# Performance work log

Hardware: AMD Instinct MI355X
Metric: run time of the kernel (lower is better)

Reference implementation:

```python
import jax, jax.numpy as jnp
import numpy as np

B, S, H, I = 2, 2048, 4096, 11008  # batch, seq, hidden_size, intermediate_size (Llama-7B)


def setup_inputs() -> dict:
    key = jax.random.key(0)
    ks = jax.random.split(key, 11)
    # int8 activations and weights (SmoothQuant W8A8)
    hidden_states = jax.random.randint(ks[0], (B, S, H), -128, 128, dtype=jnp.int8)
    w_gate = jax.random.randint(ks[1], (I, H), -128, 128, dtype=jnp.int8)
    w_up = jax.random.randint(ks[2], (I, H), -128, 128, dtype=jnp.int8)
    w_down = jax.random.randint(ks[3], (H, I), -128, 128, dtype=jnp.int8)
    # dequant scales (alpha = input_scale * weight_scale), small positive
    gate_a = jax.random.uniform(ks[4], (1,), dtype=jnp.float32) * 1e-4 + 1e-5
    up_a = jax.random.uniform(ks[5], (1,), dtype=jnp.float32) * 1e-4 + 1e-5
    down_a = jax.random.uniform(ks[6], (1,), dtype=jnp.float32) * 1e-4 + 1e-5
    # fp32 biases
    gate_b = jax.random.normal(ks[7], (I,), dtype=jnp.float32) * 0.01
    up_b = jax.random.normal(ks[8], (I,), dtype=jnp.float32) * 0.01
    down_b = jax.random.normal(ks[9], (H,), dtype=jnp.float32) * 0.01
    # requantization scale for down_proj input
    down_scale = jax.random.uniform(ks[10], (1,), dtype=jnp.float32) * 0.05 + 0.01
    return {
        "hidden_states": hidden_states,
        "w_gate": w_gate, "w_up": w_up, "w_down": w_down,
        "gate_a": gate_a, "gate_b": gate_b,
        "up_a": up_a, "up_b": up_b,
        "down_a": down_a, "down_b": down_b,
        "down_scale": down_scale,
    }


def _i8_gemm(x_i8, w_i8):
    return jnp.einsum("bsk,nk->bsn", x_i8, w_i8, preferred_element_type=jnp.int32)


def reference(hidden_states, w_gate, w_up, w_down,
              gate_a, gate_b, up_a, up_b, down_a, down_b, down_scale):
    # gate_proj: W8A8 GEMM -> dequant (alpha) + fp32 bias -> fused SiLU
    g = _i8_gemm(hidden_states, w_gate).astype(jnp.float32) * gate_a[0] + gate_b
    gate_out = g * jax.nn.sigmoid(g)  # SiLU
    # up_proj: W8A8 GEMM -> dequant + fp32 bias
    up_out = _i8_gemm(hidden_states, w_up).astype(jnp.float32) * up_a[0] + up_b
    inter = gate_out * up_out
    # requantize to int8 for down_proj input
    q = jnp.clip(jnp.round(inter / down_scale[0]), -128, 127).astype(jnp.int8)
    # down_proj: W8A8 GEMM -> dequant + fp32 bias
    down_out = _i8_gemm(q, w_down).astype(jnp.float32) * down_a[0] + down_b
    return down_out  # [B, S, H] fp32
```

## Files before the change

### kernel.cpp

```cpp
#include <hip/hip_runtime.h>
#include <cstdint>


typedef int v4i  __attribute__((ext_vector_type(4)));
typedef int v16i __attribute__((ext_vector_type(16)));

typedef const void __attribute__((address_space(1)))* gas_ptr;
typedef void __attribute__((address_space(3)))* las_ptr;

static constexpr int M_TOT = 4096;
static constexpr int HDIM  = 4096;
static constexpr int IDIM  = 11008;

#define BM 128
#define BN 128
#define BK 128

__device__ __forceinline__ void pack16(const int* __restrict__ src,
                                       int8_t* __restrict__ dst, int t) {
  const int4* s = (const int4*)(src) + t * 4;
  int4 v0 = s[0], v1 = s[1], v2 = s[2], v3 = s[3];
  int p0 = (v0.x & 0xff) | ((v0.y & 0xff) << 8) | ((v0.z & 0xff) << 16) | (v0.w << 24);
  int p1 = (v1.x & 0xff) | ((v1.y & 0xff) << 8) | ((v1.z & 0xff) << 16) | (v1.w << 24);
  int p2 = (v2.x & 0xff) | ((v2.y & 0xff) << 8) | ((v2.z & 0xff) << 16) | (v2.w << 24);
  int p3 = (v3.x & 0xff) | ((v3.y & 0xff) << 8) | ((v3.z & 0xff) << 16) | (v3.w << 24);
  ((int4*)dst)[t] = make_int4(p0, p1, p2, p3);
}

static constexpr int CX = (M_TOT * HDIM) / 16;
static constexpr int CW = (IDIM * HDIM) / 16;
static constexpr int CTOT = CX + 3 * CW;

__global__ __launch_bounds__(256) void k_pack_all(
    const int* __restrict__ X32, const int* __restrict__ Wg32,
    const int* __restrict__ Wu32, const int* __restrict__ Wd32,
    int8_t* __restrict__ Xp, int8_t* __restrict__ Wgp,
    int8_t* __restrict__ Wup, int8_t* __restrict__ Wdp) {
  int t = blockIdx.x * blockDim.x + threadIdx.x;
  if (t >= CTOT) return;
  if (t < CX)               { pack16(X32,  Xp,  t); return; }
  t -= CX;
  if (t < CW)               { pack16(Wg32, Wgp, t); return; }
  t -= CW;
  if (t < CW)               { pack16(Wu32, Wup, t); return; }
  t -= CW;
  pack16(Wd32, Wdp, t);
}

__device__ __forceinline__ void async_stage_16kb(const int8_t* __restrict__ gbase,
                                                 int ld, int8_t* lds, int tid) {
#pragma unroll
  for (int it = 0; it < 4; ++it) {
    const int chunk = it * 256 + tid;
    const int row   = chunk >> 3;
    const int slot  = chunk & 7;
    const int gch   = slot ^ (row & 7);
    const int8_t* g = gbase + row * ld + gch * 16;
    int8_t* l = lds + chunk * 16;
    __builtin_amdgcn_global_load_lds((gas_ptr)g, (las_ptr)l, 16, 0, 0);
  }
}

__device__ __forceinline__ v4i frag_ld(const int8_t* lds, int row, int kc, int half) {
  const int ch  = kc + half;
  const int sch = ch ^ (row & 7);
  return *(const v4i*)(lds + row * 128 + sch * 16);
}

#define MFMA_I8(a, b, c) __builtin_amdgcn_mfma_i32_32x32x32_i8((a), (b), (c), 0, 0, 0)

__global__ __launch_bounds__(256, 2) void k_gateup(
    const int8_t* __restrict__ X,
    const int8_t* __restrict__ Wg,
    const int8_t* __restrict__ Wu,
    const float* __restrict__ gate_a, const float* __restrict__ gate_b,
    const float* __restrict__ up_a,   const float* __restrict__ up_b,
    const float* __restrict__ down_scale,
    int8_t* __restrict__ Q) {
  __shared__ __align__(16) int8_t sA[BM * BK];
  __shared__ __align__(16) int8_t sG[BN * BK];
  __shared__ __align__(16) int8_t sU[BN * BK];

  const int tid  = threadIdx.x;
  const int lane = tid & 63;
  const int wave = tid >> 6;
  const int wm   = wave >> 1;
  const int wn   = wave & 1;
  const int half = lane >> 5;
  const int ln31 = lane & 31;

  const int m0 = blockIdx.x * BM;
  const int n0 = blockIdx.y * BN;

  const int8_t* Ab = X  + (size_t)m0 * HDIM;
  const int8_t* Gb = Wg + (size_t)n0 * HDIM;
  const int8_t* Ub = Wu + (size_t)n0 * HDIM;

  v16i accG[2][2], accU[2][2];
#pragma unroll
  for (int i = 0; i < 2; ++i)
#pragma unroll
    for (int j = 0; j < 2; ++j)
#pragma unroll
      for (int e = 0; e < 16; ++e) { accG[i][j][e] = 0; accU[i][j][e] = 0; }

  const int rA = wm * 64 + ln31;
  const int rB = wn * 64 + ln31;

  for (int k0 = 0; k0 < HDIM; k0 += BK) {
    async_stage_16kb(Ab + k0, HDIM, sA, tid);
    async_stage_16kb(Gb + k0, HDIM, sG, tid);
    async_stage_16kb(Ub + k0, HDIM, sU, tid);
    __syncthreads();
#pragma unroll
    for (int kc = 0; kc < 8; kc += 2) {
      v4i a0 = frag_ld(sA, rA,      kc, half);
      v4i a1 = frag_ld(sA, rA + 32, kc, half);
      v4i g0 = frag_ld(sG, rB,      kc, half);
      v4i g1 = frag_ld(sG, rB + 32, kc, half);
      v4i u0 = frag_ld(sU, rB,      kc, half);
      v4i u1 = frag_ld(sU, rB + 32, kc, half);
      accG[0][0] = MFMA_I8(a0, g0, accG[0][0]);
      accG[0][1] = MFMA_I8(a0, g1, accG[0][1]);
      accG[1][0] = MFMA_I8(a1, g0, accG[1][0]);
      accG[1][1] = MFMA_I8(a1, g1, accG[1][1]);
      accU[0][0] = MFMA_I8(a0, u0, accU[0][0]);
      accU[0][1] = MFMA_I8(a0, u1, accU[0][1]);
      accU[1][0] = MFMA_I8(a1, u0, accU[1][0]);
      accU[1][1] = MFMA_I8(a1, u1, accU[1][1]);
    }
    __syncthreads();
  }

  const float ga = gate_a[0];
  const float ua = up_a[0];
  const float inv_ds = 1.0f / down_scale[0];

#pragma unroll
  for (int tm = 0; tm < 2; ++tm) {
#pragma unroll
    for (int tn = 0; tn < 2; ++tn) {
      const int n = n0 + wn * 64 + tn * 32 + ln31;
      const float gb = gate_b[n];
      const float ub = up_b[n];
#pragma unroll
      for (int r = 0; r < 16; ++r) {
        const int row_l = (r & 3) + 8 * (r >> 2) + 4 * half;
        const int m = m0 + wm * 64 + tm * 32 + row_l;
        const float g = (float)accG[tm][tn][r] * ga + gb;
        const float u = (float)accU[tm][tn][r] * ua + ub;
        const float sg = g / (1.0f + __expf(-g));
        const float inter = sg * u;
        float qf = rintf(inter * inv_ds);
        qf = fminf(127.0f, fmaxf(-128.0f, qf));
        Q[(size_t)m * IDIM + n] = (int8_t)qf;
      }
    }
  }
}

__global__ __launch_bounds__(256, 2) void k_down(
    const int8_t* __restrict__ Q,
    const int8_t* __restrict__ Wd,
    const float* __restrict__ down_a, const float* __restrict__ down_b,
    float* __restrict__ Out) {
  __shared__ __align__(16) int8_t sA[256 * BK];
  __shared__ __align__(16) int8_t sB[128 * BK];

  const int tid  = threadIdx.x;
  const int lane = tid & 63;
  const int wave = tid >> 6;
  const int wm   = wave >> 1;
  const int wn   = wave & 1;
  const int half = lane >> 5;
  const int ln31 = lane & 31;

  const int m0 = blockIdx.x * 256;
  const int n0 = blockIdx.y * 128;

  const int8_t* Ab = Q  + (size_t)m0 * IDIM;
  const int8_t* Bb = Wd + (size_t)n0 * IDIM;

  v16i acc[4][2];
#pragma unroll
  for (int i = 0; i < 4; ++i)
#pragma unroll
    for (int j = 0; j < 2; ++j)
#pragma unroll
      for (int e = 0; e < 16; ++e) acc[i][j][e] = 0;

  const int rA = wm * 128 + ln31;
  const int rB = wn * 64 + ln31;

  for (int k0 = 0; k0 < IDIM; k0 += BK) {
    async_stage_16kb(Ab + k0, IDIM, sA, tid);
    async_stage_16kb(Ab + (size_t)128 * IDIM + k0, IDIM, sA + 128 * BK, tid);
    async_stage_16kb(Bb + k0, IDIM, sB, tid);
    __syncthreads();
#pragma unroll
    for (int kc = 0; kc < 8; kc += 2) {
      v4i a0 = frag_ld(sA, rA,      kc, half);
      v4i a1 = frag_ld(sA, rA + 32, kc, half);
      v4i a2 = frag_ld(sA, rA + 64, kc, half);
      v4i a3 = frag_ld(sA, rA + 96, kc, half);
      v4i b0 = frag_ld(sB, rB,      kc, half);
      v4i b1 = frag_ld(sB, rB + 32, kc, half);
      acc[0][0] = MFMA_I8(a0, b0, acc[0][0]);
      acc[0][1] = MFMA_I8(a0, b1, acc[0][1]);
      acc[1][0] = MFMA_I8(a1, b0, acc[1][0]);
      acc[1][1] = MFMA_I8(a1, b1, acc[1][1]);
      acc[2][0] = MFMA_I8(a2, b0, acc[2][0]);
      acc[2][1] = MFMA_I8(a2, b1, acc[2][1]);
      acc[3][0] = MFMA_I8(a3, b0, acc[3][0]);
      acc[3][1] = MFMA_I8(a3, b1, acc[3][1]);
    }
    __syncthreads();
  }

  const float da = down_a[0];
#pragma unroll
  for (int tm = 0; tm < 4; ++tm) {
#pragma unroll
    for (int tn = 0; tn < 2; ++tn) {
      const int n = n0 + wn * 64 + tn * 32 + ln31;
      const float db = down_b[n];
#pragma unroll
      for (int r = 0; r < 16; ++r) {
        const int row_l = (r & 3) + 8 * (r >> 2) + 4 * half;
        const int m = m0 + wm * 128 + tm * 32 + row_l;
        Out[(size_t)m * HDIM + n] = (float)acc[tm][tn][r] * da + db;
      }
    }
  }
}

extern "C" void kernel_launch(void* const* d_in, const int* in_sizes, int n_in,
                              void* d_out, int out_size, void* d_ws, size_t ws_size,
                              hipStream_t stream) {
  const int* X32        = (const int*)d_in[0];
  const int* Wg32       = (const int*)d_in[1];
  const int* Wu32       = (const int*)d_in[2];
  const int* Wd32       = (const int*)d_in[3];
  const float* gate_a   = (const float*)d_in[4];
  const float* gate_b   = (const float*)d_in[5];
  const float* up_a     = (const float*)d_in[6];
  const float* up_b     = (const float*)d_in[7];
  const float* down_a   = (const float*)d_in[8];
  const float* down_b   = (const float*)d_in[9];
  const float* down_scale = (const float*)d_in[10];
  float* Out = (float*)d_out;

  const size_t nX = (size_t)M_TOT * HDIM;
  const size_t nW = (size_t)IDIM * HDIM;

  int8_t* Q   = (int8_t*)d_ws;
  int8_t* Xp  = Q   + nW;
  int8_t* Wgp = Xp  + nX;
  int8_t* Wup = Wgp + nW;
  int8_t* Wdp = Wup + nW;

  k_pack_all<<<(CTOT + 255) / 256, 256, 0, stream>>>(X32, Wg32, Wu32, Wd32,
                                                     Xp, Wgp, Wup, Wdp);

  dim3 g1(M_TOT / BM, IDIM / BN);
  k_gateup<<<g1, dim3(256), 0, stream>>>(Xp, Wgp, Wup, gate_a, gate_b, up_a, up_b,
                                         down_scale, Q);
  dim3 g2(M_TOT / 256, HDIM / 128);
  k_down<<<g2, dim3(256), 0, stream>>>(Q, Wdp, down_a, down_b, Out);
}
```

Before: 1.110 ms.

## Rewrite GEMM mainloops with 4-stage async LDS pipeline, 512-thread blocks, grid swizzle

Both int8 GEMM kernels now use 512-thread workgroups with larger tiles (256x128 for gate/up, 256x256 for down), a 4-buffer ring of 64-wide K slices in LDS prefetched three stages ahead, and a new pair-row swizzled LDS layout. Each K slice is split into two halves that interleave issuing the next global-to-LDS loads with MFMA work, with explicit s_waitcnt/s_barrier and setprio around the MFMA bursts. Block ids are remapped through a grid swizzle for L2 locality. The goal is to hide global memory latency and raise MFMA utilisation. The cost is heavier LDS use (128KB per block), more barriers, and the possibility of subtle sync mistakes.

```diff
diff --git a/kernel.cpp b/kernel.cpp
--- a/kernel.cpp
+++ b/kernel.cpp
@@ -12,9 +12,28 @@
 static constexpr int HDIM  = 4096;
 static constexpr int IDIM  = 11008;
 
-#define BM 128
-#define BN 128
-#define BK 128
+#define MFMA_I8(a, b, c) __builtin_amdgcn_mfma_i32_32x32x32_i8((a), (b), (c), 0, 0, 0)
+#define BAR()        asm volatile("s_barrier" ::: "memory")
+#define WAIT_LGKM0() asm volatile("s_waitcnt lgkmcnt(0)" ::: "memory")
+#define WAIT_VM(N)   asm volatile("s_waitcnt vmcnt(" #N ")" ::: "memory")
+#define SETPRIO(P)   __builtin_amdgcn_s_setprio(P)
+
+__device__ __forceinline__ void gload16(const int8_t* g, int8_t* l) {
+  __builtin_amdgcn_global_load_lds((gas_ptr)g, (las_ptr)l, 16, 0, 0);
+}
+
+__device__ __forceinline__ v4i frag64(const int8_t* lds, int row, int c) {
+  const int pair = row >> 1;
+  const int slot = ((c << 1) | (row & 1)) ^ (pair & 7);
+  return *(const v4i*)(lds + pair * 128 + slot * 16);
+}
+
+__device__ __forceinline__ void relmap(int rel, int& row, int& col) {
+  const int pair = rel >> 3;
+  const int sl = (rel & 7) ^ (pair & 7);
+  row = pair * 2 + (sl & 1);
+  col = (sl >> 1) * 16;
+}
 
 __device__ __forceinline__ void pack16(const int* __restrict__ src,
                                        int8_t* __restrict__ dst, int t) {
@@ -47,29 +66,7 @@
   pack16(Wd32, Wdp, t);
 }
 
-__device__ __forceinline__ void async_stage_16kb(const int8_t* __restrict__ gbase,
-                                                 int ld, int8_t* lds, int tid) {
-#pragma unroll
-  for (int it = 0; it < 4; ++it) {
-    const int chunk = it * 256 + tid;
-    const int row   = chunk >> 3;
-    const int slot  = chunk & 7;
-    const int gch   = slot ^ (row & 7);
-    const int8_t* g = gbase + row * ld + gch * 16;
-    int8_t* l = lds + chunk * 16;
-    __builtin_amdgcn_global_load_lds((gas_ptr)g, (las_ptr)l, 16, 0, 0);
-  }
-}
-
-__device__ __forceinline__ v4i frag_ld(const int8_t* lds, int row, int kc, int half) {
-  const int ch  = kc + half;
-  const int sch = ch ^ (row & 7);
-  return *(const v4i*)(lds + row * 128 + sch * 16);
-}
-
-#define MFMA_I8(a, b, c) __builtin_amdgcn_mfma_i32_32x32x32_i8((a), (b), (c), 0, 0, 0)
-
-__global__ __launch_bounds__(256, 2) void k_gateup(
+__global__ __launch_bounds__(512, 2) void k_gateup(
     const int8_t* __restrict__ X,
     const int8_t* __restrict__ Wg,
     const int8_t* __restrict__ Wu,
@@ -77,109 +74,179 @@
     const float* __restrict__ up_a,   const float* __restrict__ up_b,
     const float* __restrict__ down_scale,
     int8_t* __restrict__ Q) {
-  __shared__ __align__(16) int8_t sA[BM * BK];
-  __shared__ __align__(16) int8_t sG[BN * BK];
-  __shared__ __align__(16) int8_t sU[BN * BK];
+  __shared__ __align__(16) int8_t lds8[4 * 32768];
 
   const int tid  = threadIdx.x;
   const int lane = tid & 63;
   const int wave = tid >> 6;
-  const int wm   = wave >> 1;
-  const int wn   = wave & 1;
+  const int wm   = wave >> 2;
+  const int wn   = wave & 3;
   const int half = lane >> 5;
   const int ln31 = lane & 31;
 
-  const int m0 = blockIdx.x * BM;
-  const int n0 = blockIdx.y * BN;
+  const int NB  = IDIM / 128;
+  const int NWG = (M_TOT / 256) * NB;
+  const int id  = blockIdx.x;
+  const int swz = (id & 7) * (NWG >> 3) + (id >> 3);
+  const int m0  = (swz / NB) * 256;
+  const int n0  = (swz % NB) * 128;
 
   const int8_t* Ab = X  + (size_t)m0 * HDIM;
   const int8_t* Gb = Wg + (size_t)n0 * HDIM;
   const int8_t* Ub = Wu + (size_t)n0 * HDIM;
 
-  v16i accG[2][2], accU[2][2];
-#pragma unroll
-  for (int i = 0; i < 2; ++i)
-#pragma unroll
-    for (int j = 0; j < 2; ++j)
-#pragma unroll
-      for (int e = 0; e < 16; ++e) { accG[i][j][e] = 0; accU[i][j][e] = 0; }
-
-  const int rA = wm * 64 + ln31;
-  const int rB = wn * 64 + ln31;
-
-  for (int k0 = 0; k0 < HDIM; k0 += BK) {
-    async_stage_16kb(Ab + k0, HDIM, sA, tid);
-    async_stage_16kb(Gb + k0, HDIM, sG, tid);
-    async_stage_16kb(Ub + k0, HDIM, sU, tid);
-    __syncthreads();
-#pragma unroll
-    for (int kc = 0; kc < 8; kc += 2) {
-      v4i a0 = frag_ld(sA, rA,      kc, half);
-      v4i a1 = frag_ld(sA, rA + 32, kc, half);
-      v4i g0 = frag_ld(sG, rB,      kc, half);
-      v4i g1 = frag_ld(sG, rB + 32, kc, half);
-      v4i u0 = frag_ld(sU, rB,      kc, half);
-      v4i u1 = frag_ld(sU, rB + 32, kc, half);
-      accG[0][0] = MFMA_I8(a0, g0, accG[0][0]);
-      accG[0][1] = MFMA_I8(a0, g1, accG[0][1]);
-      accG[1][0] = MFMA_I8(a1, g0, accG[1][0]);
-      accG[1][1] = MFMA_I8(a1, g1, accG[1][1]);
-      accU[0][0] = MFMA_I8(a0, u0, accU[0][0]);
-      accU[0][1] = MFMA_I8(a0, u1, accU[0][1]);
-      accU[1][0] = MFMA_I8(a1, u0, accU[1][0]);
-      accU[1][1] = MFMA_I8(a1, u1, accU[1][1]);
-    }
-    __syncthreads();
+  int r0, c0, r1, c1;
+  relmap(tid, r0, c0);
+  relmap(tid + 512, r1, c1);
+  const size_t offA0 = (size_t)r0 * HDIM + c0;
+  const size_t offA1 = (size_t)r1 * HDIM + c1;
+  const size_t offW  = offA0;
+  const int ldsA0 = tid * 16;
+  const int ldsA1 = (tid + 512) * 16;
+  const int ldsG  = 16384 + tid * 16;
+  const int ldsU  = 24576 + tid * 16;
+
+  v16i accG[4], accU[4];
+#pragma unroll
+  for (int i = 0; i < 4; ++i)
+#pragma unroll
+    for (int e = 0; e < 16; ++e) { accG[i][e] = 0; accU[i][e] = 0; }
+
+  const int rA = wm * 128 + ln31;
+  const int rB = wn * 32 + ln31;
+
+#pragma unroll
+  for (int pt = 0; pt < 3; ++pt) {
+    int8_t* sb = &lds8[pt * 32768];
+    const size_t ks = (size_t)pt * 64;
+    gload16(Ab + ks + offA0, sb + ldsA0);
+    gload16(Ab + ks + offA1, sb + ldsA1);
+    gload16(Gb + ks + offW,  sb + ldsG);
+    gload16(Ub + ks + offW,  sb + ldsU);
+  }
+  WAIT_VM(8);
+  BAR();
+
+  const int NT = HDIM / 64;
+  for (int t = 0; t < NT; ++t) {
+    const int8_t* bufA = &lds8[(t & 3) * 32768];
+    const int8_t* bufG = bufA + 16384;
+    const int8_t* bufU = bufA + 24576;
+    int8_t* sb = &lds8[((t + 3) & 3) * 32768];
+    const size_t ks = (size_t)(t + 3) * 64;
+    const bool st = (t + 3 < NT);
+
+    {
+      v4i a0 = frag64(bufA, rA,      half);
+      v4i a1 = frag64(bufA, rA + 32, half);
+      v4i a2 = frag64(bufA, rA + 64, half);
+      v4i a3 = frag64(bufA, rA + 96, half);
+      v4i gg = frag64(bufG, rB, half);
+      v4i uu = frag64(bufU, rB, half);
+      if (st) {
+        gload16(Ab + ks + offA0, sb + ldsA0);
+        gload16(Ab + ks + offA1, sb + ldsA1);
+      }
+      BAR();
+      WAIT_LGKM0();
+      SETPRIO(1);
+      accG[0] = MFMA_I8(a0, gg, accG[0]);
+      accU[0] = MFMA_I8(a0, uu, accU[0]);
+      accG[1] = MFMA_I8(a1, gg, accG[1]);
+      accU[1] = MFMA_I8(a1, uu, accU[1]);
+      accG[2] = MFMA_I8(a2, gg, accG[2]);
+      accU[2] = MFMA_I8(a2, uu, accU[2]);
+      accG[3] = MFMA_I8(a3, gg, accG[3]);
+      accU[3] = MFMA_I8(a3, uu, accU[3]);
+      SETPRIO(0);
+      BAR();
+    }
+    {
+      v4i a0 = frag64(bufA, rA,      2 + half);
+      v4i a1 = frag64(bufA, rA + 32, 2 + half);
+      v4i a2 = frag64(bufA, rA + 64, 2 + half);
+      v4i a3 = frag64(bufA, rA + 96, 2 + half);
+      v4i gg = frag64(bufG, rB, 2 + half);
+      v4i uu = frag64(bufU, rB, 2 + half);
+      if (st) {
+        gload16(Gb + ks + offW, sb + ldsG);
+        gload16(Ub + ks + offW, sb + ldsU);
+      }
+      BAR();
+      WAIT_LGKM0();
+      SETPRIO(1);
+      accG[0] = MFMA_I8(a0, gg, accG[0]);
+      accU[0] = MFMA_I8(a0, uu, accU[0]);
+      accG[1] = MFMA_I8(a1, gg, accG[1]);
+      accU[1] = MFMA_I8(a1, uu, accU[1]);
+      accG[2] = MFMA_I8(a2, gg, accG[2]);
+      accU[2] = MFMA_I8(a2, uu, accU[2]);
+      accG[3] = MFMA_I8(a3, gg, accG[3]);
+      accU[3] = MFMA_I8(a3, uu, accU[3]);
+      SETPRIO(0);
+      if (t + 3 < NT)      { WAIT_VM(8); }
+      else if (t + 2 < NT) { WAIT_VM(4); }
+      else if (t + 1 < NT) { WAIT_VM(0); }
+      BAR();
+    }
   }
 
   const float ga = gate_a[0];
   const float ua = up_a[0];
   const float inv_ds = 1.0f / down_scale[0];
-
-#pragma unroll
-  for (int tm = 0; tm < 2; ++tm) {
-#pragma unroll
-    for (int tn = 0; tn < 2; ++tn) {
-      const int n = n0 + wn * 64 + tn * 32 + ln31;
-      const float gb = gate_b[n];
-      const float ub = up_b[n];
-#pragma unroll
-      for (int r = 0; r < 16; ++r) {
-        const int row_l = (r & 3) + 8 * (r >> 2) + 4 * half;
-        const int m = m0 + wm * 64 + tm * 32 + row_l;
-        const float g = (float)accG[tm][tn][r] * ga + gb;
-        const float u = (float)accU[tm][tn][r] * ua + ub;
-        const float sg = g / (1.0f + __expf(-g));
-        const float inter = sg * u;
-        float qf = rintf(inter * inv_ds);
-        qf = fminf(127.0f, fmaxf(-128.0f, qf));
-        Q[(size_t)m * IDIM + n] = (int8_t)qf;
-      }
-    }
-  }
-}
-
-__global__ __launch_bounds__(256, 2) void k_down(
-    const int8_t* __restrict__ Q,
+  const int n = n0 + wn * 32 + ln31;
+  const float gb = gate_b[n];
+  const float ub = up_b[n];
+
+#pragma unroll
+  for (int tm = 0; tm < 4; ++tm) {
+#pragma unroll
+    for (int r = 0; r < 16; ++r) {
+      const int row_l = (r & 3) + 8 * (r >> 2) + 4 * half;
+      const int m = m0 + wm * 128 + tm * 32 + row_l;
+      const float g = (float)accG[tm][r] * ga + gb;
+      const float u = (float)accU[tm][r] * ua + ub;
+      const float sg = g / (1.0f + __expf(-g));
+      const float inter = sg * u;
+      float qf = rintf(inter * inv_ds);
+      qf = fminf(127.0f, fmaxf(-128.0f, qf));
+      Q[(size_t)m * IDIM + n] = (int8_t)qf;
+    }
+  }
+}
+
+__global__ __launch_bounds__(512, 2) void k_down(
+    const int8_t* __restrict__ Qm,
     const int8_t* __restrict__ Wd,
     const float* __restrict__ down_a, const float* __restrict__ down_b,
     float* __restrict__ Out) {
-  __shared__ __align__(16) int8_t sA[256 * BK];
-  __shared__ __align__(16) int8_t sB[128 * BK];
+  __shared__ __align__(16) int8_t lds8[4 * 32768];
 
   const int tid  = threadIdx.x;
   const int lane = tid & 63;
   const int wave = tid >> 6;
-  const int wm   = wave >> 1;
-  const int wn   = wave & 1;
+  const int wm   = wave >> 2;
+  const int wn   = wave & 3;
   const int half = lane >> 5;
   const int ln31 = lane & 31;
 
-  const int m0 = blockIdx.x * 256;
-  const int n0 = blockIdx.y * 128;
-
-  const int8_t* Ab = Q  + (size_t)m0 * IDIM;
+  const int id  = blockIdx.x;
+  const int swz = (id & 7) * 32 + (id >> 3);
+  const int m0  = (swz >> 4) * 256;
+  const int n0  = (swz & 15) * 256;
+
+  const int8_t* Ab = Qm + (size_t)m0 * IDIM;
   const int8_t* Bb = Wd + (size_t)n0 * IDIM;
+
+  int r0, c0, r1, c1;
+  relmap(tid, r0, c0);
+  relmap(tid + 512, r1, c1);
+  const size_t off0 = (size_t)r0 * IDIM + c0;
+  const size_t off1 = (size_t)r1 * IDIM + c1;
+  const int ldsA0 = tid * 16;
+  const int ldsA1 = (tid + 512) * 16;
+  const int ldsB0 = 16384 + tid * 16;
+  const int ldsB1 = 16384 + (tid + 512) * 16;
 
   v16i acc[4][2];
 #pragma unroll
@@ -192,19 +259,40 @@
   const int rA = wm * 128 + ln31;
   const int rB = wn * 64 + ln31;
 
-  for (int k0 = 0; k0 < IDIM; k0 += BK) {
-    async_stage_16kb(Ab + k0, IDIM, sA, tid);
-    async_stage_16kb(Ab + (size_t)128 * IDIM + k0, IDIM, sA + 128 * BK, tid);
-    async_stage_16kb(Bb + k0, IDIM, sB, tid);
-    __syncthreads();
-#pragma unroll
-    for (int kc = 0; kc < 8; kc += 2) {
-      v4i a0 = frag_ld(sA, rA,      kc, half);
-      v4i a1 = frag_ld(sA, rA + 32, kc, half);
-      v4i a2 = frag_ld(sA, rA + 64, kc, half);
-      v4i a3 = frag_ld(sA, rA + 96, kc, half);
-      v4i b0 = frag_ld(sB, rB,      kc, half);
-      v4i b1 = frag_ld(sB, rB + 32, kc, half);
+#pragma unroll
+  for (int pt = 0; pt < 3; ++pt) {
+    int8_t* sb = &lds8[pt * 32768];
+    const size_t ks = (size_t)pt * 64;
+    gload16(Ab + ks + off0, sb + ldsA0);
+    gload16(Ab + ks + off1, sb + ldsA1);
+    gload16(Bb + ks + off0, sb + ldsB0);
+    gload16(Bb + ks + off1, sb + ldsB1);
+  }
+  WAIT_VM(8);
+  BAR();
+
+  const int NT = IDIM / 64;
+  for (int t = 0; t < NT; ++t) {
+    const int8_t* bufA = &lds8[(t & 3) * 32768];
+    const int8_t* bufB = bufA + 16384;
+    int8_t* sb = &lds8[((t + 3) & 3) * 32768];
+    const size_t ks = (size_t)(t + 3) * 64;
+    const bool st = (t + 3 < NT);
+
+    {
+      v4i a0 = frag64(bufA, rA,      half);
+      v4i a1 = frag64(bufA, rA + 32, half);
+      v4i a2 = frag64(bufA, rA + 64, half);
+      v4i a3 = frag64(bufA, rA + 96, half);
+      v4i b0 = frag64(bufB, rB,      half);
+      v4i b1 = frag64(bufB, rB + 32, half);
+      if (st) {
+        gload16(Ab + ks + off0, sb + ldsA0);
+        gload16(Ab + ks + off1, sb + ldsA1);
+      }
+      BAR();
+      WAIT_LGKM0();
+      SETPRIO(1);
       acc[0][0] = MFMA_I8(a0, b0, acc[0][0]);
       acc[0][1] = MFMA_I8(a0, b1, acc[0][1]);
       acc[1][0] = MFMA_I8(a1, b0, acc[1][0]);
@@ -213,17 +301,46 @@
       acc[2][1] = MFMA_I8(a2, b1, acc[2][1]);
       acc[3][0] = MFMA_I8(a3, b0, acc[3][0]);
       acc[3][1] = MFMA_I8(a3, b1, acc[3][1]);
-    }
-    __syncthreads();
+      SETPRIO(0);
+      BAR();
+    }
+    {
+      v4i a0 = frag64(bufA, rA,      2 + half);
+      v4i a1 = frag64(bufA, rA + 32, 2 + half);
+      v4i a2 = frag64(bufA, rA + 64, 2 + half);
+      v4i a3 = frag64(bufA, rA + 96, 2 + half);
+      v4i b0 = frag64(bufB, rB,      2 + half);
+      v4i b1 = frag64(bufB, rB + 32, 2 + half);
+      if (st) {
+        gload16(Bb + ks + off0, sb + ldsB0);
+        gload16(Bb + ks + off1, sb + ldsB1);
+      }
+      BAR();
+      WAIT_LGKM0();
+      SETPRIO(1);
+      acc[0][0] = MFMA_I8(a0, b0, acc[0][0]);
+      acc[0][1] = MFMA_I8(a0, b1, acc[0][1]);
+      acc[1][0] = MFMA_I8(a1, b0, acc[1][0]);
+      acc[1][1] = MFMA_I8(a1, b1, acc[1][1]);
+      acc[2][0] = MFMA_I8(a2, b0, acc[2][0]);
+      acc[2][1] = MFMA_I8(a2, b1, acc[2][1]);
+      acc[3][0] = MFMA_I8(a3, b0, acc[3][0]);
+      acc[3][1] = MFMA_I8(a3, b1, acc[3][1]);
+      SETPRIO(0);
+      if (t + 3 < NT)      { WAIT_VM(8); }
+      else if (t + 2 < NT) { WAIT_VM(4); }
+      else if (t + 1 < NT) { WAIT_VM(0); }
+      BAR();
+    }
   }
 
   const float da = down_a[0];
 #pragma unroll
-  for (int tm = 0; tm < 4; ++tm) {
-#pragma unroll
-    for (int tn = 0; tn < 2; ++tn) {
-      const int n = n0 + wn * 64 + tn * 32 + ln31;
-      const float db = down_b[n];
+  for (int tn = 0; tn < 2; ++tn) {
+    const int n = n0 + wn * 64 + tn * 32 + ln31;
+    const float db = down_b[n];
+#pragma unroll
+    for (int tm = 0; tm < 4; ++tm) {
 #pragma unroll
       for (int r = 0; r < 16; ++r) {
         const int row_l = (r & 3) + 8 * (r >> 2) + 4 * half;
@@ -262,9 +379,9 @@
   k_pack_all<<<(CTOT + 255) / 256, 256, 0, stream>>>(X32, Wg32, Wu32, Wd32,
                                                      Xp, Wgp, Wup, Wdp);
 
-  dim3 g1(M_TOT / BM, IDIM / BN);
-  k_gateup<<<g1, dim3(256), 0, stream>>>(Xp, Wgp, Wup, gate_a, gate_b, up_a, up_b,
-                                         down_scale, Q);
-  dim3 g2(M_TOT / 256, HDIM / 128);
-  k_down<<<g2, dim3(256), 0, stream>>>(Q, Wdp, down_a, down_b, Out);
-}
+  k_gateup<<<dim3((M_TOT / 256) * (IDIM / 128)), dim3(512), 0, stream>>>(
+      Xp, Wgp, Wup, gate_a, gate_b, up_a, up_b, down_scale, Q);
+
+  k_down<<<dim3((M_TOT / 256) * (HDIM / 256)), dim3(512), 0, stream>>>(
+      Q, Wdp, down_a, down_b, Out);
+}
```

After: 1.121 ms. No clear change (+0.9%).

## Double-buffer LDS with 512-thread blocks, larger tiles, new swizzle in both GEMMs

Applied to the files above, without the earlier changes.

Both int8 GEMM kernels now use 512-thread blocks with larger output tiles (256x128 for gate/up, 256x256 for down) and double-buffered 128 KB LDS. The next K-tile's global-to-LDS loads are issued before the MFMAs on the current tile. The LDS layout switches to a row-pair XOR swizzle, and MFMA issue priority is raised during compute. The aim is to hide global load latency, raise data reuse per tile and cut bank conflicts, at the cost of heavy LDS use that limits occupancy to one block per CU.

```diff
diff --git a/kernel.cpp b/kernel.cpp
--- a/kernel.cpp
+++ b/kernel.cpp
@@ -12,9 +12,27 @@
 static constexpr int HDIM  = 4096;
 static constexpr int IDIM  = 11008;
 
-#define BM 128
-#define BN 128
-#define BK 128
+#define MFMA_I8(a, b, c) __builtin_amdgcn_mfma_i32_32x32x32_i8((a), (b), (c), 0, 0, 0)
+#define BAR()      asm volatile("s_barrier" ::: "memory")
+#define WAIT_VM0() asm volatile("s_waitcnt vmcnt(0)" ::: "memory")
+#define SETPRIO(P) __builtin_amdgcn_s_setprio(P)
+
+__device__ __forceinline__ void gload16(const int8_t* g, int8_t* l) {
+  __builtin_amdgcn_global_load_lds((gas_ptr)g, (las_ptr)l, 16, 0, 0);
+}
+
+__device__ __forceinline__ v4i frag128(const int8_t* lds, int row, int c) {
+  const int pair = row >> 1;
+  const int slot = ((c << 1) | (row & 1)) ^ (pair & 15);
+  return *(const v4i*)(lds + pair * 256 + slot * 16);
+}
+
+__device__ __forceinline__ void relmap128(int rel, int& row, int& col) {
+  const int pair = rel >> 4;
+  const int sl = (rel & 15) ^ (pair & 15);
+  row = 2 * pair + (sl & 1);
+  col = (sl >> 1) * 16;
+}
 
 __device__ __forceinline__ void pack16(const int* __restrict__ src,
                                        int8_t* __restrict__ dst, int t) {
@@ -47,29 +65,7 @@
   pack16(Wd32, Wdp, t);
 }
 
-__device__ __forceinline__ void async_stage_16kb(const int8_t* __restrict__ gbase,
-                                                 int ld, int8_t* lds, int tid) {
-#pragma unroll
-  for (int it = 0; it < 4; ++it) {
-    const int chunk = it * 256 + tid;
-    const int row   = chunk >> 3;
-    const int slot  = chunk & 7;
-    const int gch   = slot ^ (row & 7);
-    const int8_t* g = gbase + row * ld + gch * 16;
-    int8_t* l = lds + chunk * 16;
-    __builtin_amdgcn_global_load_lds((gas_ptr)g, (las_ptr)l, 16, 0, 0);
-  }
-}
-
-__device__ __forceinline__ v4i frag_ld(const int8_t* lds, int row, int kc, int half) {
-  const int ch  = kc + half;
-  const int sch = ch ^ (row & 7);
-  return *(const v4i*)(lds + row * 128 + sch * 16);
-}
-
-#define MFMA_I8(a, b, c) __builtin_amdgcn_mfma_i32_32x32x32_i8((a), (b), (c), 0, 0, 0)
-
-__global__ __launch_bounds__(256, 2) void k_gateup(
+__global__ __launch_bounds__(512, 2) void k_gateup(
     const int8_t* __restrict__ X,
     const int8_t* __restrict__ Wg,
     const int8_t* __restrict__ Wu,
@@ -77,109 +73,158 @@
     const float* __restrict__ up_a,   const float* __restrict__ up_b,
     const float* __restrict__ down_scale,
     int8_t* __restrict__ Q) {
-  __shared__ __align__(16) int8_t sA[BM * BK];
-  __shared__ __align__(16) int8_t sG[BN * BK];
-  __shared__ __align__(16) int8_t sU[BN * BK];
+  __shared__ __align__(16) int8_t lds8[2 * 65536];
 
   const int tid  = threadIdx.x;
   const int lane = tid & 63;
   const int wave = tid >> 6;
-  const int wm   = wave >> 1;
-  const int wn   = wave & 1;
+  const int wm   = wave >> 2;
+  const int wn   = wave & 3;
   const int half = lane >> 5;
   const int ln31 = lane & 31;
 
-  const int m0 = blockIdx.x * BM;
-  const int n0 = blockIdx.y * BN;
+  const int m0 = blockIdx.x * 256;
+  const int n0 = blockIdx.y * 128;
 
   const int8_t* Ab = X  + (size_t)m0 * HDIM;
   const int8_t* Gb = Wg + (size_t)n0 * HDIM;
   const int8_t* Ub = Wu + (size_t)n0 * HDIM;
 
-  v16i accG[2][2], accU[2][2];
-#pragma unroll
-  for (int i = 0; i < 2; ++i)
-#pragma unroll
-    for (int j = 0; j < 2; ++j)
-#pragma unroll
-      for (int e = 0; e < 16; ++e) { accG[i][j][e] = 0; accU[i][j][e] = 0; }
-
-  const int rA = wm * 64 + ln31;
-  const int rB = wn * 64 + ln31;
-
-  for (int k0 = 0; k0 < HDIM; k0 += BK) {
-    async_stage_16kb(Ab + k0, HDIM, sA, tid);
-    async_stage_16kb(Gb + k0, HDIM, sG, tid);
-    async_stage_16kb(Ub + k0, HDIM, sU, tid);
-    __syncthreads();
-#pragma unroll
-    for (int kc = 0; kc < 8; kc += 2) {
-      v4i a0 = frag_ld(sA, rA,      kc, half);
-      v4i a1 = frag_ld(sA, rA + 32, kc, half);
-      v4i g0 = frag_ld(sG, rB,      kc, half);
-      v4i g1 = frag_ld(sG, rB + 32, kc, half);
-      v4i u0 = frag_ld(sU, rB,      kc, half);
-      v4i u1 = frag_ld(sU, rB + 32, kc, half);
-      accG[0][0] = MFMA_I8(a0, g0, accG[0][0]);
-      accG[0][1] = MFMA_I8(a0, g1, accG[0][1]);
-      accG[1][0] = MFMA_I8(a1, g0, accG[1][0]);
-      accG[1][1] = MFMA_I8(a1, g1, accG[1][1]);
-      accU[0][0] = MFMA_I8(a0, u0, accU[0][0]);
-      accU[0][1] = MFMA_I8(a0, u1, accU[0][1]);
-      accU[1][0] = MFMA_I8(a1, u0, accU[1][0]);
-      accU[1][1] = MFMA_I8(a1, u1, accU[1][1]);
-    }
-    __syncthreads();
+  int r0, c0, r1, c1, r2, c2, r3, c3;
+  relmap128(tid,        r0, c0);
+  relmap128(tid + 512,  r1, c1);
+  relmap128(tid + 1024, r2, c2);
+  relmap128(tid + 1536, r3, c3);
+  const size_t oA0 = (size_t)r0 * HDIM + c0;
+  const size_t oA1 = (size_t)r1 * HDIM + c1;
+  const size_t oA2 = (size_t)r2 * HDIM + c2;
+  const size_t oA3 = (size_t)r3 * HDIM + c3;
+
+  v16i accG[4], accU[4];
+#pragma unroll
+  for (int i = 0; i < 4; ++i)
+#pragma unroll
+    for (int e = 0; e < 16; ++e) { accG[i][e] = 0; accU[i][e] = 0; }
+
+  const int rA = wm * 128 + ln31;
+  const int rB = wn * 32 + ln31;
+
+  {
+    int8_t* sb = lds8;
+    gload16(Ab + oA0, sb + tid * 16);
+    gload16(Ab + oA1, sb + (tid + 512) * 16);
+    gload16(Ab + oA2, sb + (tid + 1024) * 16);
+    gload16(Ab + oA3, sb + (tid + 1536) * 16);
+    gload16(Gb + oA0, sb + 32768 + tid * 16);
+    gload16(Gb + oA1, sb + 32768 + (tid + 512) * 16);
+    gload16(Ub + oA0, sb + 49152 + tid * 16);
+    gload16(Ub + oA1, sb + 49152 + (tid + 512) * 16);
+    WAIT_VM0();
+    BAR();
+  }
+
+  const int NT = HDIM / 128;
+  for (int s = 0; s < NT; ++s) {
+    const int8_t* bufA = lds8 + (s & 1) * 65536;
+    const int8_t* bufG = bufA + 32768;
+    const int8_t* bufU = bufA + 49152;
+
+    if (s + 1 < NT) {
+      int8_t* sb = lds8 + ((s + 1) & 1) * 65536;
+      const int8_t* ap = Ab + (size_t)(s + 1) * 128;
+      const int8_t* gp = Gb + (size_t)(s + 1) * 128;
+      const int8_t* up = Ub + (size_t)(s + 1) * 128;
+      gload16(ap + oA0, sb + tid * 16);
+      gload16(ap + oA1, sb + (tid + 512) * 16);
+      gload16(ap + oA2, sb + (tid + 1024) * 16);
+      gload16(ap + oA3, sb + (tid + 1536) * 16);
+      gload16(gp + oA0, sb + 32768 + tid * 16);
+      gload16(gp + oA1, sb + 32768 + (tid + 512) * 16);
+      gload16(up + oA0, sb + 49152 + tid * 16);
+      gload16(up + oA1, sb + 49152 + (tid + 512) * 16);
+    }
+
+    SETPRIO(1);
+#pragma unroll
+    for (int ks = 0; ks < 4; ++ks) {
+      const int c = 2 * ks + half;
+      v4i a0 = frag128(bufA, rA,      c);
+      v4i a1 = frag128(bufA, rA + 32, c);
+      v4i a2 = frag128(bufA, rA + 64, c);
+      v4i a3 = frag128(bufA, rA + 96, c);
+      v4i gg = frag128(bufG, rB, c);
+      v4i uu = frag128(bufU, rB, c);
+      accG[0] = MFMA_I8(a0, gg, accG[0]);
+      accU[0] = MFMA_I8(a0, uu, accU[0]);
+      accG[1] = MFMA_I8(a1, gg, accG[1]);
+      accU[1] = MFMA_I8(a1, uu, accU[1]);
+      accG[2] = MFMA_I8(a2, gg, accG[2]);
+      accU[2] = MFMA_I8(a2, uu, accU[2]);
+      accG[3] = MFMA_I8(a3, gg, accG[3]);
+      accU[3] = MFMA_I8(a3, uu, accU[3]);
+    }
+    SETPRIO(0);
+
+    if (s + 1 < NT) {
+      WAIT_VM0();
+      BAR();
+    }
   }
 
   const float ga = gate_a[0];
   const float ua = up_a[0];
   const float inv_ds = 1.0f / down_scale[0];
-
-#pragma unroll
-  for (int tm = 0; tm < 2; ++tm) {
-#pragma unroll
-    for (int tn = 0; tn < 2; ++tn) {
-      const int n = n0 + wn * 64 + tn * 32 + ln31;
-      const float gb = gate_b[n];
-      const float ub = up_b[n];
-#pragma unroll
-      for (int r = 0; r < 16; ++r) {
-        const int row_l = (r & 3) + 8 * (r >> 2) + 4 * half;
-        const int m = m0 + wm * 64 + tm * 32 + row_l;
-        const float g = (float)accG[tm][tn][r] * ga + gb;
-        const float u = (float)accU[tm][tn][r] * ua + ub;
-        const float sg = g / (1.0f + __expf(-g));
-        const float inter = sg * u;
-        float qf = rintf(inter * inv_ds);
-        qf = fminf(127.0f, fmaxf(-128.0f, qf));
-        Q[(size_t)m * IDIM + n] = (int8_t)qf;
-      }
-    }
-  }
-}
-
-__global__ __launch_bounds__(256, 2) void k_down(
-    const int8_t* __restrict__ Q,
+  const int n = n0 + wn * 32 + ln31;
+  const float gb = gate_b[n];
+  const float ub = up_b[n];
+
+#pragma unroll
+  for (int tm = 0; tm < 4; ++tm) {
+#pragma unroll
+    for (int r = 0; r < 16; ++r) {
+      const int row_l = (r & 3) + 8 * (r >> 2) + 4 * half;
+      const int m = m0 + wm * 128 + tm * 32 + row_l;
+      const float g = (float)accG[tm][r] * ga + gb;
+      const float u = (float)accU[tm][r] * ua + ub;
+      const float sg = g / (1.0f + __expf(-g));
+      const float inter = sg * u;
+      float qf = rintf(inter * inv_ds);
+      qf = fminf(127.0f, fmaxf(-128.0f, qf));
+      Q[(size_t)m * IDIM + n] = (int8_t)qf;
+    }
+  }
+}
+
+__global__ __launch_bounds__(512, 2) void k_down(
+    const int8_t* __restrict__ Qm,
     const int8_t* __restrict__ Wd,
     const float* __restrict__ down_a, const float* __restrict__ down_b,
     float* __restrict__ Out) {
-  __shared__ __align__(16) int8_t sA[256 * BK];
-  __shared__ __align__(16) int8_t sB[128 * BK];
+  __shared__ __align__(16) int8_t lds8[2 * 65536];
 
   const int tid  = threadIdx.x;
   const int lane = tid & 63;
   const int wave = tid >> 6;
-  const int wm   = wave >> 1;
-  const int wn   = wave & 1;
+  const int wm   = wave >> 2;
+  const int wn   = wave & 3;
   const int half = lane >> 5;
   const int ln31 = lane & 31;
 
   const int m0 = blockIdx.x * 256;
-  const int n0 = blockIdx.y * 128;
-
-  const int8_t* Ab = Q  + (size_t)m0 * IDIM;
+  const int n0 = blockIdx.y * 256;
+
+  const int8_t* Ab = Qm + (size_t)m0 * IDIM;
   const int8_t* Bb = Wd + (size_t)n0 * IDIM;
+
+  int r0, c0, r1, c1, r2, c2, r3, c3;
+  relmap128(tid,        r0, c0);
+  relmap128(tid + 512,  r1, c1);
+  relmap128(tid + 1024, r2, c2);
+  relmap128(tid + 1536, r3, c3);
+  const size_t o0 = (size_t)r0 * IDIM + c0;
+  const size_t o1 = (size_t)r1 * IDIM + c1;
+  const size_t o2 = (size_t)r2 * IDIM + c2;
+  const size_t o3 = (size_t)r3 * IDIM + c3;
 
   v16i acc[4][2];
 #pragma unroll
@@ -192,19 +237,49 @@
   const int rA = wm * 128 + ln31;
   const int rB = wn * 64 + ln31;
 
-  for (int k0 = 0; k0 < IDIM; k0 += BK) {
-    async_stage_16kb(Ab + k0, IDIM, sA, tid);
-    async_stage_16kb(Ab + (size_t)128 * IDIM + k0, IDIM, sA + 128 * BK, tid);
-    async_stage_16kb(Bb + k0, IDIM, sB, tid);
-    __syncthreads();
-#pragma unroll
-    for (int kc = 0; kc < 8; kc += 2) {
-      v4i a0 = frag_ld(sA, rA,      kc, half);
-      v4i a1 = frag_ld(sA, rA + 32, kc, half);
-      v4i a2 = frag_ld(sA, rA + 64, kc, half);
-      v4i a3 = frag_ld(sA, rA + 96, kc, half);
-      v4i b0 = frag_ld(sB, rB,      kc, half);
-      v4i b1 = frag_ld(sB, rB + 32, kc, half);
+  {
+    int8_t* sb = lds8;
+    gload16(Ab + o0, sb + tid * 16);
+    gload16(Ab + o1, sb + (tid + 512) * 16);
+    gload16(Ab + o2, sb + (tid + 1024) * 16);
+    gload16(Ab + o3, sb + (tid + 1536) * 16);
+    gload16(Bb + o0, sb + 32768 + tid * 16);
+    gload16(Bb + o1, sb + 32768 + (tid + 512) * 16);
+    gload16(Bb + o2, sb + 32768 + (tid + 1024) * 16);
+    gload16(Bb + o3, sb + 32768 + (tid + 1536) * 16);
+    WAIT_VM0();
+    BAR();
+  }
+
+  const int NT = IDIM / 128;
+  for (int s = 0; s < NT; ++s) {
+    const int8_t* bufA = lds8 + (s & 1) * 65536;
+    const int8_t* bufB = bufA + 32768;
+
+    if (s + 1 < NT) {
+      int8_t* sb = lds8 + ((s + 1) & 1) * 65536;
+      const int8_t* ap = Ab + (size_t)(s + 1) * 128;
+      const int8_t* bp = Bb + (size_t)(s + 1) * 128;
+      gload16(ap + o0, sb + tid * 16);
+      gload16(ap + o1, sb + (tid + 512) * 16);
+      gload16(ap + o2, sb + (tid + 1024) * 16);
+      gload16(ap + o3, sb + (tid + 1536) * 16);
+      gload16(bp + o0, sb + 32768 + tid * 16);
+      gload16(bp + o1, sb + 32768 + (tid + 512) * 16);
+      gload16(bp + o2, sb + 32768 + (tid + 1024) * 16);
+      gload16(bp + o3, sb + 32768 + (tid + 1536) * 16);
+    }
+
+    SETPRIO(1);
+#pragma unroll
+    for (int ks = 0; ks < 4; ++ks) {
+      const int c = 2 * ks + half;
+      v4i a0 = frag128(bufA, rA,      c);
+      v4i a1 = frag128(bufA, rA + 32, c);
+      v4i a2 = frag128(bufA, rA + 64, c);
+      v4i a3 = frag128(bufA, rA + 96, c);
+      v4i b0 = frag128(bufB, rB,      c);
+      v4i b1 = frag128(bufB, rB + 32, c);
       acc[0][0] = MFMA_I8(a0, b0, acc[0][0]);
       acc[0][1] = MFMA_I8(a0, b1, acc[0][1]);
       acc[1][0] = MFMA_I8(a1, b0, acc[1][0]);
@@ -214,16 +289,21 @@
       acc[3][0] = MFMA_I8(a3, b0, acc[3][0]);
       acc[3][1] = MFMA_I8(a3, b1, acc[3][1]);
     }
-    __syncthreads();
+    SETPRIO(0);
+
+    if (s + 1 < NT) {
+      WAIT_VM0();
+      BAR();
+    }
   }
 
   const float da = down_a[0];
 #pragma unroll
-  for (int tm = 0; tm < 4; ++tm) {
-#pragma unroll
-    for (int tn = 0; tn < 2; ++tn) {
-      const int n = n0 + wn * 64 + tn * 32 + ln31;
-      const float db = down_b[n];
+  for (int tn = 0; tn < 2; ++tn) {
+    const int n = n0 + wn * 64 + tn * 32 + ln31;
+    const float db = down_b[n];
+#pragma unroll
+    for (int tm = 0; tm < 4; ++tm) {
 #pragma unroll
       for (int r = 0; r < 16; ++r) {
         const int row_l = (r & 3) + 8 * (r >> 2) + 4 * half;
@@ -262,9 +342,9 @@
   k_pack_all<<<(CTOT + 255) / 256, 256, 0, stream>>>(X32, Wg32, Wu32, Wd32,
                                                      Xp, Wgp, Wup, Wdp);
 
-  dim3 g1(M_TOT / BM, IDIM / BN);
-  k_gateup<<<g1, dim3(256), 0, stream>>>(Xp, Wgp, Wup, gate_a, gate_b, up_a, up_b,
-                                         down_scale, Q);
-  dim3 g2(M_TOT / 256, HDIM / 128);
-  k_down<<<g2, dim3(256), 0, stream>>>(Q, Wdp, down_a, down_b, Out);
-}
+  k_gateup<<<dim3(M_TOT / 256, IDIM / 128), dim3(512), 0, stream>>>(
+      Xp, Wgp, Wup, gate_a, gate_b, up_a, up_b, down_scale, Q);
+
+  k_down<<<dim3(M_TOT / 256, HDIM / 256), dim3(512), 0, stream>>>(
+      Q, Wdp, down_a, down_b, Out);
+}
```

Measured after the change: 1.092 ms. Within noise of the previous version (-1.7%).
